# Kernel tuning notes

Hardware: AMD Instinct MI355X
Metric: run time of the kernel (lower is better)

The kernel has to match this reference:

```python
import jax, jax.numpy as jnp
import numpy as np

B, P, K, F, H = 128, 200, 60, 4, 64   # events, points/event, knn k, feat dim, hidden
N = B * P


def setup_inputs() -> dict:
    key = jax.random.key(0)
    k0, k1, k2, k3 = jax.random.split(key, 4)
    x = jax.random.normal(k0, (N, F), jnp.float32)
    pos = jax.random.normal(k1, (N, 3), jnp.float32)
    batch = jnp.arange(N, dtype=jnp.int32) // P  # sorted event ids, equal-size events
    W1 = jax.random.normal(k2, (F + 3, H), jnp.float32) / np.sqrt(F + 3)
    b1 = jnp.zeros((H,), jnp.float32)
    W2 = jax.random.normal(k3, (H, H), jnp.float32) / np.sqrt(H)
    b2 = jnp.zeros((H,), jnp.float32)
    return {"x": x, "pos": pos, "batch": batch, "W1": W1, "b1": b1, "W2": W2, "b2": b2}


def _knn_edges(pos):
    """knn_graph(pos, K, batch, loop=False, flow='source_to_target').
    Equal-size events -> batched [B,P,P] pairwise distances, no cross-event edges."""
    p = pos.reshape(B, P, 3)
    d2 = jnp.sum((p[:, :, None, :] - p[:, None, :, :]) ** 2, axis=-1)  # [B,P,P]
    d2 = d2 + jnp.eye(P, dtype=d2.dtype) * 1e10                        # exclude self (loop=False)
    _, nbr = jax.lax.top_k(-d2, K)                                     # [B,P,K] local neighbor ids
    src = (nbr + (jnp.arange(B, dtype=nbr.dtype) * P)[:, None, None]).reshape(-1)  # sources j
    dst = jnp.repeat(jnp.arange(N, dtype=src.dtype), K)                             # targets i
    return jnp.stack([src, dst])  # [2, N*K]


def _local_nn(m, W1, b1, W2, b2):
    h = jax.nn.relu(m @ W1 + b1)
    return jax.nn.relu(h @ W2 + b2)


def reference(x, pos, batch, W1, b1, W2, b2):
    edge_index = _knn_edges(pos)
    src, dst = edge_index[0], edge_index[1]
    # PointConv message: net(concat[x_j, pos_j - pos_i]) on each edge
    rel = pos[src] - pos[dst]                             # [E,3]
    m = jnp.concatenate([x[src], rel], axis=-1)           # [E,F+3]
    h = _local_nn(m, W1, b1, W2, b2)                      # [E,H]
    out = h.reshape(N, K, H).max(axis=1)                  # max-aggregate per target node
    # PyG PointConv adds self-loops by default: message with rel = 0
    m_self = jnp.concatenate([x, jnp.zeros((N, 3), x.dtype)], axis=-1)
    h_self = _local_nn(m_self, W1, b1, W2, b2)            # [N,H]
    out = jnp.maximum(out, h_self)
    return (out, pos, batch, edge_index)
```

## Files before the change

kernel.cpp:

```cpp
#include <hip/hip_runtime.h>
#include <hip/hip_bf16.h>

typedef unsigned int u32;
typedef unsigned long long u64;
typedef __attribute__((ext_vector_type(8))) short bf16x8;
typedef __attribute__((ext_vector_type(4))) float f32x4;
typedef __attribute__((ext_vector_type(4))) u32 u32x4;

#define NB 128
#define PP 200
#define KK 60
#define NN (NB*PP)
#define HH 64
#define TW 2
#define NWV 5
#define TB (TW*NWV)
#define BPE (PP/TB)
#define NTHREADS (NWV*64)

#define OUT_OFF   0
#define POS_OFF   (NN*HH)
#define BATCH_OFF (POS_OFF + NN*3)
#define ESRC_OFF  (BATCH_OFF + NN)
#define EDST_OFF  (ESRC_OFF + NN*KK)

static __device__ __forceinline__ u32 packtr(float a, float b) {
    return __builtin_amdgcn_perm(__float_as_uint(b), __float_as_uint(a), 0x07060302u);
}
static __device__ __forceinline__ u32 prefix_lt(u64 b) {
    return __builtin_amdgcn_mbcnt_hi((u32)(b >> 32),
                                     __builtin_amdgcn_mbcnt_lo((u32)b, 0));
}
static __device__ __forceinline__ float wavemax16(float v) {
    u32 x = __float_as_uint(v);
    auto p16 = __builtin_amdgcn_permlane16_swap(x, x, false, false);
    float m = fmaxf(__uint_as_float(p16[0]), __uint_as_float(p16[1]));
    u32 y = __float_as_uint(m);
    auto p32 = __builtin_amdgcn_permlane32_swap(y, y, false, false);
    return fmaxf(__uint_as_float(p32[0]), __uint_as_float(p32[1]));
}

__global__ __launch_bounds__(NTHREADS) void fused_kernel(const float* __restrict__ x,
                                                    const float* __restrict__ pos,
                                                    const float* __restrict__ W1,
                                                    const float* __restrict__ b1p,
                                                    const float* __restrict__ W2,
                                                    const float* __restrict__ b2p,
                                                    float* __restrict__ out) {
    __shared__ alignas(16) float xs[PP * 4];
    __shared__ alignas(16) float psl[PP * 3];
    __shared__ alignas(16) u32 jslot[NWV * TW * 64];
    __shared__ alignas(16) u32 msg[NWV * TW * 256];
    __shared__ alignas(16) u32 pkW1[64 * 4];
    __shared__ alignas(16) u32 pkW2T[64 * 33];
    __shared__ alignas(16) float b2s[64];
    __shared__ alignas(16) u32 zrow[4];

    int tid = threadIdx.x, blk = blockIdx.x;
    int e = blk / BPE;
    int pl0b = (blk % BPE) * TB;
    int i0b  = e * PP + pl0b;

    if (tid < 3*TB) out[POS_OFF + i0b * 3 + tid] = pos[i0b * 3 + tid];
    if (tid < TB)   out[BATCH_OFF + i0b + tid] = (float)e;

    if (tid < 200) ((f32x4*)xs)[tid]  = ((const f32x4*)x)[e * PP + tid];
    if (tid < 150) ((f32x4*)psl)[tid] = ((const f32x4*)pos)[e * 150 + tid];
    if (tid < 4)   zrow[tid] = 0u;

    if (tid < 256) {
        int m = tid & 63, d = tid >> 6;
        float hiv = (d < 3) ? W1[(2*d + 1)*64 + m] : b1p[m];
        pkW1[m*4 + d] = packtr(W1[(2*d)*64 + m], hiv);
    }
    #pragma unroll
    for (int r = 0; r < 4; ++r) {
        int g = r * NTHREADS + tid;
        if (g < 1024) {
            int kp = g >> 4, colq = g & 15;
            f32x4 ra = *(const f32x4*)&W2[(2*kp)    *64 + colq*4];
            f32x4 rb = *(const f32x4*)&W2[(2*kp + 1)*64 + colq*4];
            #pragma unroll
            for (int c = 0; c < 4; ++c)
                pkW2T[(colq*4 + c)*33 + kp] = packtr(ra[c], rb[c]);
        }
    }
    if (tid < 64) b2s[tid] = b2p[tid];
    __syncthreads();

    int lane = tid & 63, wv = tid >> 6;
    int lo16 = lane & 15, hi16 = lane >> 4;
    int plW0 = pl0b + wv * TW;
    int iW0  = e * PP + plW0;

    u32 key[TW][4];
    {
        float ax[TW], ay[TW], az[TW];
        #pragma unroll
        for (int t = 0; t < TW; ++t) {
            ax[t] = psl[(plW0+t)*3]; ay[t] = psl[(plW0+t)*3+1]; az[t] = psl[(plW0+t)*3+2];
        }
        #pragma unroll
        for (int q = 0; q < 4; ++q) {
            int j = lane + q * 64;
            int jc = (j < PP) ? j : 0;
            float px = psl[jc*3], py = psl[jc*3+1], pz = psl[jc*3+2];
            #pragma unroll
            for (int t = 0; t < TW; ++t) {
                float dx = px-ax[t], dy = py-ay[t], dz = pz-az[t];
                float d2 = dx*dx + dy*dy + dz*dz;
                key[t][q] = (j < PP && j != plW0 + t)
                          ? ((__float_as_uint(d2) & 0xFFFFFF00u) | (u32)j) : 0xFFFFFFFFu;
            }
        }
    }

    u32 lo[TW], hi[TW]; int done[TW];
    #pragma unroll
    for (int t = 0; t < TW; ++t) { lo[t] = 0u; hi[t] = 0x7F800000u; done[t] = 0; }
    #pragma unroll 1
    for (int it = 0; it < 40; ++it) {
        #pragma unroll
        for (int t = 0; t < TW; ++t) {
            if (!done[t]) {
                u32 m = lo[t] + ((hi[t] - lo[t]) >> 1);
                int c = __builtin_popcountll(__ballot(key[t][0] < m))
                      + __builtin_popcountll(__ballot(key[t][1] < m))
                      + __builtin_popcountll(__ballot(key[t][2] < m))
                      + __builtin_popcountll(__ballot(key[t][3] < m));
                if (c >= KK) hi[t] = m; else lo[t] = m;
                done[t] = (c == KK) | (hi[t] - lo[t] <= 1u);
            }
        }
        int alldone = done[0];
        #pragma unroll
        for (int t = 1; t < TW; ++t) alldone &= done[t];
        if (alldone) break;
    }

    const int jsb = wv * (TW * 64);
    #pragma unroll
    for (int t = 0; t < TW; ++t) {
        if (lane >= KK) jslot[jsb + t * 64 + lane] = (u32)(plW0 + t);
        u64 m0 = __ballot(key[t][0] < hi[t]);
        u64 m1 = __ballot(key[t][1] < hi[t]);
        u64 m2 = __ballot(key[t][2] < hi[t]);
        u64 m3 = __ballot(key[t][3] < hi[t]);
        u32 s1 = (u32)__builtin_popcountll(m0);
        u32 s2 = s1 + (u32)__builtin_popcountll(m1);
        u32 s3 = s2 + (u32)__builtin_popcountll(m2);
        u32 sl[4] = { prefix_lt(m0), s1 + prefix_lt(m1),
                      s2 + prefix_lt(m2), s3 + prefix_lt(m3) };
        #pragma unroll
        for (int q = 0; q < 4; ++q)
            if (key[t][q] < hi[t]) jslot[jsb + t * 64 + (int)sl[q]] = key[t][q] & 0xFFu;
    }
    #pragma unroll
    for (int t = 0; t < TW; ++t) {
        int i = iW0 + t;
        if (lane < KK) {
            out[ESRC_OFF + i * KK + lane] = (float)(e * PP + (int)jslot[jsb + t * 64 + lane]);
            out[EDST_OFF + i * KK + lane] = (float)i;
        }
    }

    bf16x8 w1f[4];
    #pragma unroll
    for (int th = 0; th < 4; ++th) {
        union { u32 w[4]; bf16x8 v; } u;
        if (hi16 == 0) *(u32x4*)u.w = *(const u32x4*)&pkW1[(th * 16 + lo16) * 4];
        else { u.w[0] = u.w[1] = u.w[2] = u.w[3] = 0u; }
        w1f[th] = u.v;
    }
    bf16x8 bfr[4][2];
    #pragma unroll
    for (int t = 0; t < 4; ++t)
        #pragma unroll
        for (int s = 0; s < 2; ++s) {
            union { u32 w[4]; bf16x8 v; } u;
            int base = (t * 16 + lo16) * 33 + s * 16 + hi16 * 4;
            #pragma unroll
            for (int d = 0; d < 4; ++d) u.w[d] = pkW2T[base + d];
            bfr[t][s] = u.v;
        }
    float b2me = b2s[lane];

    const int msb = wv * (TW * 256);
    #pragma unroll
    for (int tl = 0; tl < TW; ++tl) {
        int pl = plW0 + tl;
        int jloc = (int)jslot[jsb + tl * 64 + lane];
        f32x4 xv = ((const f32x4*)xs)[jloc];
        float rx = psl[jloc*3]   - psl[pl*3];
        float ry = psl[jloc*3+1] - psl[pl*3+1];
        float rz = psl[jloc*3+2] - psl[pl*3+2];
        u32x4 mrow;
        mrow[0] = packtr(xv[0], xv[1]);
        mrow[1] = packtr(xv[2], xv[3]);
        mrow[2] = packtr(rx, ry);
        mrow[3] = packtr(rz, 1.0f);
        *(u32x4*)&msg[msb + tl * 256 + lane * 4] = mrow;
    }

    #pragma unroll
    for (int tl = 0; tl < TW; ++tl) {
        int i = iW0 + tl;
        const u32* mbase = (hi16 == 0) ? &msg[msb + tl * 256 + lo16 * 4] : zrow;
        const int mstep  = (hi16 == 0) ? 64 : 0;

        float rmax[4] = {-3.0e38f, -3.0e38f, -3.0e38f, -3.0e38f};
        __builtin_amdgcn_s_setprio(1);
        #pragma unroll
        for (int rt = 0; rt < 4; ++rt) {
            union { u32 w[4]; bf16x8 v; } mu;
            *(u32x4*)mu.w = *(const u32x4*)(mbase + rt * mstep);

            f32x4 c1[4];
            #pragma unroll
            for (int th = 0; th < 4; ++th)
                c1[th] = __builtin_amdgcn_mfma_f32_16x16x32_bf16(w1f[th], mu.v,
                                                                 (f32x4)0.f, 0, 0, 0);
            f32x4 acc[4];
            #pragma unroll
            for (int t = 0; t < 4; ++t) acc[t] = (f32x4)0.f;

            #pragma unroll
            for (int s = 0; s < 2; ++s) {
                u32 pe0 = packtr(fmaxf(c1[2*s][0], 0.f), fmaxf(c1[2*s][1], 0.f));
                u32 pe1 = packtr(fmaxf(c1[2*s][2], 0.f), fmaxf(c1[2*s][3], 0.f));
                u32 po0 = packtr(fmaxf(c1[2*s+1][0], 0.f), fmaxf(c1[2*s+1][1], 0.f));
                u32 po1 = packtr(fmaxf(c1[2*s+1][2], 0.f), fmaxf(c1[2*s+1][3], 0.f));
                union { u32 w[4]; bf16x8 v; } u;
                {
                    auto t0 = __builtin_amdgcn_permlane32_swap(pe0, po0, false, false);
                    auto w0 = __builtin_amdgcn_permlane16_swap(t0[0], t0[1], false, false);
                    u.w[0] = w0[0]; u.w[2] = w0[1];
                }
                {
                    auto t1 = __builtin_amdgcn_permlane32_swap(pe1, po1, false, false);
                    auto w1 = __builtin_amdgcn_permlane16_swap(t1[0], t1[1], false, false);
                    u.w[1] = w1[0]; u.w[3] = w1[1];
                }
                #pragma unroll
                for (int t = 0; t < 4; ++t)
                    acc[t] = __builtin_amdgcn_mfma_f32_16x16x32_bf16(u.v, bfr[t][s],
                                                                     acc[t], 0, 0, 0);
            }
            #pragma unroll
            for (int t = 0; t < 4; ++t) {
                rmax[t] = fmaxf(fmaxf(acc[t][0], acc[t][1]), rmax[t]);
                rmax[t] = fmaxf(fmaxf(acc[t][2], acc[t][3]), rmax[t]);
            }
        }
        __builtin_amdgcn_s_setprio(0);
        #pragma unroll
        for (int t = 0; t < 4; ++t) rmax[t] = wavemax16(rmax[t]);
        float sel = rmax[0];
        sel = (hi16 == 1) ? rmax[1] : sel;
        sel = (hi16 == 2) ? rmax[2] : sel;
        sel = (hi16 == 3) ? rmax[3] : sel;
        out[OUT_OFF + i * 64 + lane] = fmaxf(sel + b2me, 0.f);
    }
}

extern "C" void kernel_launch(void* const* d_in, const int* in_sizes, int n_in,
                              void* d_out, int out_size, void* d_ws, size_t ws_size,
                              hipStream_t stream) {
    const float* x     = (const float*)d_in[0];
    const float* pos   = (const float*)d_in[1];
    const float* W1    = (const float*)d_in[3];
    const float* b1    = (const float*)d_in[4];
    const float* W2    = (const float*)d_in[5];
    const float* b2    = (const float*)d_in[6];
    float* out = (float*)d_out;
    (void)d_ws; (void)ws_size; (void)in_sizes; (void)n_in; (void)out_size;

    fused_kernel<<<dim3(NN / TB), dim3(NTHREADS), 0, stream>>>(x, pos, W1, b1, W2, b2, out);
}
```

Measured before the change: 127.2 us.

## Use 4-wave blocks, pre-pack x to bf16, unroll bisection, hoist weight loads

Shrinks each block from five waves to four (8 targets per block), which also removes the thread-count guards on the weight packing. The x features are converted to bf16 pairs once when staged into shared memory. The kNN bisection loop is unrolled by four with predicated updates instead of branches. MFMA weight-fragment loads and edge-dst stores are moved before the selection, and the message buffer is reused per target instead of holding both at once. Together these aim to cut per-block overhead, branch divergence and LDS footprint, but they change block count and occupancy and may run extra bisection steps.

Result: faster. 113.7 us (-10.6%).

```diff
diff --git a/kernel.cpp b/kernel.cpp
--- a/kernel.cpp
+++ b/kernel.cpp
@@ -6,6 +6,7 @@
 typedef __attribute__((ext_vector_type(8))) short bf16x8;
 typedef __attribute__((ext_vector_type(4))) float f32x4;
 typedef __attribute__((ext_vector_type(4))) u32 u32x4;
+typedef __attribute__((ext_vector_type(2))) u32 u32x2;
 
 #define NB 128
 #define PP 200
@@ -13,7 +14,7 @@
 #define NN (NB*PP)
 #define HH 64
 #define TW 2
-#define NWV 5
+#define NWV 4
 #define TB (TW*NWV)
 #define BPE (PP/TB)
 #define NTHREADS (NWV*64)
@@ -47,10 +48,10 @@
                                                     const float* __restrict__ W2,
                                                     const float* __restrict__ b2p,
                                                     float* __restrict__ out) {
-    __shared__ alignas(16) float xs[PP * 4];
+    __shared__ alignas(16) u32 xsp[PP * 2];
     __shared__ alignas(16) float psl[PP * 3];
     __shared__ alignas(16) u32 jslot[NWV * TW * 64];
-    __shared__ alignas(16) u32 msg[NWV * TW * 256];
+    __shared__ alignas(16) u32 msg[NWV * 256];
     __shared__ alignas(16) u32 pkW1[64 * 4];
     __shared__ alignas(16) u32 pkW2T[64 * 33];
     __shared__ alignas(16) float b2s[64];
@@ -64,11 +65,15 @@
     if (tid < 3*TB) out[POS_OFF + i0b * 3 + tid] = pos[i0b * 3 + tid];
     if (tid < TB)   out[BATCH_OFF + i0b + tid] = (float)e;
 
-    if (tid < 200) ((f32x4*)xs)[tid]  = ((const f32x4*)x)[e * PP + tid];
+    if (tid < 200) {
+        f32x4 xv = ((const f32x4*)x)[e * PP + tid];
+        u32x2 p; p[0] = packtr(xv[0], xv[1]); p[1] = packtr(xv[2], xv[3]);
+        *(u32x2*)&xsp[tid * 2] = p;
+    }
     if (tid < 150) ((f32x4*)psl)[tid] = ((const f32x4*)pos)[e * 150 + tid];
     if (tid < 4)   zrow[tid] = 0u;
 
-    if (tid < 256) {
+    {
         int m = tid & 63, d = tid >> 6;
         float hiv = (d < 3) ? W1[(2*d + 1)*64 + m] : b1p[m];
         pkW1[m*4 + d] = packtr(W1[(2*d)*64 + m], hiv);
@@ -76,14 +81,12 @@
     #pragma unroll
     for (int r = 0; r < 4; ++r) {
         int g = r * NTHREADS + tid;
-        if (g < 1024) {
-            int kp = g >> 4, colq = g & 15;
-            f32x4 ra = *(const f32x4*)&W2[(2*kp)    *64 + colq*4];
-            f32x4 rb = *(const f32x4*)&W2[(2*kp + 1)*64 + colq*4];
-            #pragma unroll
-            for (int c = 0; c < 4; ++c)
-                pkW2T[(colq*4 + c)*33 + kp] = packtr(ra[c], rb[c]);
-        }
+        int kp = g >> 4, colq = g & 15;
+        f32x4 ra = *(const f32x4*)&W2[(2*kp)    *64 + colq*4];
+        f32x4 rb = *(const f32x4*)&W2[(2*kp + 1)*64 + colq*4];
+        #pragma unroll
+        for (int c = 0; c < 4; ++c)
+            pkW2T[(colq*4 + c)*33 + kp] = packtr(ra[c], rb[c]);
     }
     if (tid < 64) b2s[tid] = b2p[tid];
     __syncthreads();
@@ -92,6 +95,10 @@
     int lo16 = lane & 15, hi16 = lane >> 4;
     int plW0 = pl0b + wv * TW;
     int iW0  = e * PP + plW0;
+
+    #pragma unroll
+    for (int t = 0; t < TW; ++t)
+        if (lane < KK) out[EDST_OFF + (iW0 + t) * KK + lane] = (float)(iW0 + t);
 
     u32 key[TW][4];
     {
@@ -115,21 +122,46 @@
         }
     }
 
+    bf16x8 w1f[4];
+    #pragma unroll
+    for (int th = 0; th < 4; ++th) {
+        union { u32 w[4]; bf16x8 v; } u;
+        if (hi16 == 0) *(u32x4*)u.w = *(const u32x4*)&pkW1[(th * 16 + lo16) * 4];
+        else { u.w[0] = u.w[1] = u.w[2] = u.w[3] = 0u; }
+        w1f[th] = u.v;
+    }
+    bf16x8 bfr[4][2];
+    #pragma unroll
+    for (int t = 0; t < 4; ++t)
+        #pragma unroll
+        for (int s = 0; s < 2; ++s) {
+            union { u32 w[4]; bf16x8 v; } u;
+            int base = (t * 16 + lo16) * 33 + s * 16 + hi16 * 4;
+            #pragma unroll
+            for (int d = 0; d < 4; ++d) u.w[d] = pkW2T[base + d];
+            bfr[t][s] = u.v;
+        }
+    float b2me = b2s[lane];
+
     u32 lo[TW], hi[TW]; int done[TW];
     #pragma unroll
     for (int t = 0; t < TW; ++t) { lo[t] = 0u; hi[t] = 0x7F800000u; done[t] = 0; }
     #pragma unroll 1
-    for (int it = 0; it < 40; ++it) {
-        #pragma unroll
-        for (int t = 0; t < TW; ++t) {
-            if (!done[t]) {
+    for (int g = 0; g < 8; ++g) {
+        #pragma unroll
+        for (int u4 = 0; u4 < 4; ++u4) {
+            #pragma unroll
+            for (int t = 0; t < TW; ++t) {
                 u32 m = lo[t] + ((hi[t] - lo[t]) >> 1);
                 int c = __builtin_popcountll(__ballot(key[t][0] < m))
                       + __builtin_popcountll(__ballot(key[t][1] < m))
                       + __builtin_popcountll(__ballot(key[t][2] < m))
                       + __builtin_popcountll(__ballot(key[t][3] < m));
-                if (c >= KK) hi[t] = m; else lo[t] = m;
-                done[t] = (c == KK) | (hi[t] - lo[t] <= 1u);
+                int upd = !done[t];
+                int ge  = (c >= KK);
+                hi[t] = (upd & ge)  ? m : hi[t];
+                lo[t] = (upd & !ge) ? m : lo[t];
+                done[t] |= (c == KK) | (hi[t] - lo[t] <= 1u);
             }
         }
         int alldone = done[0];
@@ -158,55 +190,27 @@
     #pragma unroll
     for (int t = 0; t < TW; ++t) {
         int i = iW0 + t;
-        if (lane < KK) {
+        if (lane < KK)
             out[ESRC_OFF + i * KK + lane] = (float)(e * PP + (int)jslot[jsb + t * 64 + lane]);
-            out[EDST_OFF + i * KK + lane] = (float)i;
-        }
-    }
-
-    bf16x8 w1f[4];
-    #pragma unroll
-    for (int th = 0; th < 4; ++th) {
-        union { u32 w[4]; bf16x8 v; } u;
-        if (hi16 == 0) *(u32x4*)u.w = *(const u32x4*)&pkW1[(th * 16 + lo16) * 4];
-        else { u.w[0] = u.w[1] = u.w[2] = u.w[3] = 0u; }
-        w1f[th] = u.v;
-    }
-    bf16x8 bfr[4][2];
-    #pragma unroll
-    for (int t = 0; t < 4; ++t)
-        #pragma unroll
-        for (int s = 0; s < 2; ++s) {
-            union { u32 w[4]; bf16x8 v; } u;
-            int base = (t * 16 + lo16) * 33 + s * 16 + hi16 * 4;
-            #pragma unroll
-            for (int d = 0; d < 4; ++d) u.w[d] = pkW2T[base + d];
-            bfr[t][s] = u.v;
-        }
-    float b2me = b2s[lane];
-
-    const int msb = wv * (TW * 256);
-    #pragma unroll
+    }
+
+    const int msb = wv * 256;
+    const u32* mbase = (hi16 == 0) ? &msg[msb + lo16 * 4] : zrow;
+    const int mstep  = (hi16 == 0) ? 64 : 0;
+
     for (int tl = 0; tl < TW; ++tl) {
-        int pl = plW0 + tl;
+        int i = iW0 + tl, pl = plW0 + tl;
         int jloc = (int)jslot[jsb + tl * 64 + lane];
-        f32x4 xv = ((const f32x4*)xs)[jloc];
+        u32x2 xp = *(const u32x2*)&xsp[jloc * 2];
         float rx = psl[jloc*3]   - psl[pl*3];
         float ry = psl[jloc*3+1] - psl[pl*3+1];
         float rz = psl[jloc*3+2] - psl[pl*3+2];
         u32x4 mrow;
-        mrow[0] = packtr(xv[0], xv[1]);
-        mrow[1] = packtr(xv[2], xv[3]);
+        mrow[0] = xp[0];
+        mrow[1] = xp[1];
         mrow[2] = packtr(rx, ry);
         mrow[3] = packtr(rz, 1.0f);
-        *(u32x4*)&msg[msb + tl * 256 + lane * 4] = mrow;
-    }
-
-    #pragma unroll
-    for (int tl = 0; tl < TW; ++tl) {
-        int i = iW0 + tl;
-        const u32* mbase = (hi16 == 0) ? &msg[msb + tl * 256 + lo16 * 4] : zrow;
-        const int mstep  = (hi16 == 0) ? 64 : 0;
+        *(u32x4*)&msg[msb + lane * 4] = mrow;
 
         float rmax[4] = {-3.0e38f, -3.0e38f, -3.0e38f, -3.0e38f};
         __builtin_amdgcn_s_setprio(1);
```
